# Kernel optimization log

Measured on AMD Instinct MI355X. Metric: run time of the kernel, lower is better.

The kernel has to match this reference:

```python
import jax, jax.numpy as jnp
import numpy as np
from jax import lax

B, CIN, COUT, K, S, P, H, W = 8, 128, 256, 3, 1, 1, 64, 64


def setup_inputs() -> dict:
    key = jax.random.key(0)
    k1, k2, k3, k4, k5 = jax.random.split(key, 5)
    fan_off = CIN * K * K
    fan_dc = CIN * K * K
    return {
        "x": jax.random.normal(k1, (B, CIN, H, W), dtype=jnp.float32),
        # offset-predicting conv: Conv2d(CIN, 2*K*K, K, S, P, padding_mode='reflect')
        "w_off": jax.random.normal(k2, (2 * K * K, CIN, K, K), dtype=jnp.float32) / np.sqrt(fan_off),
        "b_off": jax.random.normal(k3, (2 * K * K,), dtype=jnp.float32) * 0.01,
        # deformable conv weights: DeformConv2d(CIN, COUT, K, S, P)
        "w_dc": jax.random.normal(k4, (COUT, CIN, K, K), dtype=jnp.float32) / np.sqrt(fan_dc),
        "b_dc": jax.random.normal(k5, (COUT,), dtype=jnp.float32) * 0.01,
    }


def _reflect_conv(x, w, b, stride, pad):
    # Conv2d with reflect padding
    xp = jnp.pad(x, ((0, 0), (0, 0), (pad, pad), (pad, pad)), mode="reflect")
    y = lax.conv_general_dilated(xp, w, (stride, stride), "VALID",
                                 dimension_numbers=("NCHW", "OIHW", "NCHW"))
    return y + b[None, :, None, None]


def _deform_conv(x, offset, w, b, k, stride, pad):
    # torchvision DeformConv2d (v1, no mask, 1 offset group)
    Bn, C, Hi, Wi = x.shape
    Ho, Wo = offset.shape[2], offset.shape[3]
    KK = k * k
    # offset layout: [B, 2*KK, Ho, Wo], interleaved (dy, dx) per kernel position
    off = offset.reshape(Bn, KK, 2, Ho, Wo)
    hb = jnp.arange(Ho, dtype=x.dtype) * stride - pad          # base rows
    wb = jnp.arange(Wo, dtype=x.dtype) * stride - pad          # base cols
    ki, kj = jnp.meshgrid(jnp.arange(k, dtype=x.dtype), jnp.arange(k, dtype=x.dtype), indexing="ij")
    ki, kj = ki.reshape(KK), kj.reshape(KK)
    # sampling locations [B, KK, Ho, Wo]
    py = off[:, :, 0] + hb[None, None, :, None] + ki[None, :, None, None]
    px = off[:, :, 1] + wb[None, None, None, :] + kj[None, :, None, None]
    y0 = jnp.floor(py)
    x0 = jnp.floor(px)
    dy = (py - y0).reshape(Bn, 1, -1)
    dx = (px - x0).reshape(Bn, 1, -1)
    y0i = y0.astype(jnp.int32)
    x0i = x0.astype(jnp.int32)
    xf = x.reshape(Bn, C, Hi * Wi)

    def gather(yi, xi):
        valid = (yi >= 0) & (yi < Hi) & (xi >= 0) & (xi < Wi)
        yc = jnp.clip(yi, 0, Hi - 1)
        xc = jnp.clip(xi, 0, Wi - 1)
        idx = (yc * Wi + xc).reshape(Bn, -1)                   # [B, KK*Ho*Wo]
        g = jax.vmap(lambda xb, ib: xb[:, ib])(xf, idx)        # [B, C, KK*Ho*Wo]
        return g * valid.reshape(Bn, 1, -1).astype(x.dtype)

    v00 = gather(y0i, x0i)
    v01 = gather(y0i, x0i + 1)
    v10 = gather(y0i + 1, x0i)
    v11 = gather(y0i + 1, x0i + 1)
    vals = (v00 * (1 - dy) * (1 - dx) + v01 * (1 - dy) * dx
            + v10 * dy * (1 - dx) + v11 * dy * dx)             # [B, C, KK*Ho*Wo]
    cols = vals.reshape(Bn, C, KK, Ho * Wo)
    out = jnp.einsum("bckl,ock->bol", cols, w.reshape(-1, C, KK))
    out = out + b[None, :, None]
    return out.reshape(Bn, -1, Ho, Wo)


def reference(x, w_off, b_off, w_dc, b_dc):
    x_offset = _reflect_conv(x, w_off, b_off, S, P)            # [B, 2*K*K, Ho, Wo]
    # torch.chunk followed by torch.concat is an identity on the offset tensor
    return _deform_conv(x, x_offset, w_dc, b_dc, K, S, P)
```

## Files before the change

### kernel.cpp

```cpp
#include <hip/hip_runtime.h>
#include <hip/hip_fp16.h>

typedef unsigned short u16;
typedef unsigned int   u32;
typedef u32   u32x2  __attribute__((ext_vector_type(2)));
typedef u32   u32x4  __attribute__((ext_vector_type(4)));
typedef short short8 __attribute__((ext_vector_type(8)));
typedef float f32x4  __attribute__((ext_vector_type(4)));
typedef _Float16 half8 __attribute__((ext_vector_type(8)));

__device__ __forceinline__ u16 f2h(float f) { return __half_as_ushort(__float2half(f)); }
__device__ __forceinline__ f32x4 mfma16(short8 a, short8 b, f32x4 c) {
  return __builtin_amdgcn_mfma_f32_16x16x32_f16(
      __builtin_bit_cast(half8, a), __builtin_bit_cast(half8, b), c, 0, 0, 0);
}
__device__ __forceinline__ __half2 h2cast(u32 u) { return __builtin_bit_cast(__half2, u); }
__device__ __forceinline__ int refl(int v) { return v < 0 ? -v : (v > 63 ? 126 - v : v); }

__device__ __forceinline__ void softbar() {
  asm volatile("s_waitcnt lgkmcnt(0)" ::: "memory");
  __builtin_amdgcn_s_barrier();
  asm volatile("" ::: "memory");
}

__global__ __launch_bounds__(256) void prep_fused(const float* __restrict__ x,
                                                  const float* __restrict__ w_dc,
                                                  const float* __restrict__ w_off,
                                                  u16* __restrict__ xh,
                                                  u16* __restrict__ Wl2,
                                                  u16* __restrict__ Wol2) {
  int bid = blockIdx.x;
  int tid = threadIdx.x;
  if (bid < 512) {
    __shared__ float tile[128][65];
    int swz = (bid & 7) * 64 + (bid >> 3);
    int b = swz >> 6, h = swz & 63;
    for (int i = 0; i < 32; ++i) {
      int c = (tid >> 6) + i * 4;
      int w = tid & 63;
      tile[c][w] = x[(((size_t)b * 128 + c) * 64 + h) * 64 + w];
    }
    __syncthreads();
    u16* dst = xh + ((size_t)(b * 64 + h) * 64) * 128;
    for (int j = 0; j < 32; ++j) {
      int c = tid & 127;
      int w = (tid >> 7) + 2 * j;
      dst[w * 128 + c] = f2h(tile[c][w]);
    }
  } else {
    int idx = (bid - 512) * 256 + tid;
    if (idx < 294912) {
      int e = idx & 7, lane = (idx >> 3) & 63, ks = (idx >> 9) & 3;
      int mt = (idx >> 11) & 15, kk = idx >> 15;
      int o = mt * 16 + (lane & 15), c = ks * 32 + (lane >> 4) * 8 + e;
      Wl2[idx] = f2h(w_dc[(o * 128 + c) * 9 + kk]);
    } else {
      int i2 = idx - 294912;
      int e = i2 & 7, lane = (i2 >> 3) & 63, ks = (i2 >> 9) & 3;
      int mt = (i2 >> 11) & 1, kk = i2 >> 12;
      int co = mt * 16 + (lane & 15), c = ks * 32 + (lane >> 4) * 8 + e;
      Wol2[i2] = (co < 18) ? f2h(w_off[(co * 128 + c) * 9 + kk]) : (u16)0;
    }
  }
}

__device__ __forceinline__ void make_entry_lds(u32x4* __restrict__ tbl, int kk,
                                               int ho, int wo, float offy, float offx) {
  int ki = kk / 3, kj = kk - ki * 3;
  float py = offy + (float)(ho + ki - 1);
  float px = offx + (float)(wo + kj - 1);
  float fy0 = floorf(py), fx0 = floorf(px);
  int y0 = (int)fy0, x0 = (int)fx0;
  float fy = py - fy0, fx = px - fx0;
  float w11 = fy * fx, w10 = fy - w11, w01 = fx - w11, w00 = 1.f - fy - fx + w11;
  bool iy0 = (y0 >= 0) & (y0 < 64), iy1 = (y0 >= -1) & (y0 < 63);
  bool ix0 = (x0 >= 0) & (x0 < 64), ix1 = (x0 >= -1) & (x0 < 63);
  int y0c = min(max(y0, 0), 63), x0c = min(max(x0, 0), 63);
  u32 addr00 = (u32)((y0c * 64 + x0c) * 128);
  u32 dx = (x0 >= 0 && x0 < 63) ? 128u : 0u;
  u32 dy = (y0 >= 0 && y0 < 63) ? 8192u : 0u;
  u32 wA = (u32)f2h((iy0 && ix0) ? w00 : 0.f) | ((u32)f2h((iy0 && ix1) ? w01 : 0.f) << 16);
  u32 wB = (u32)f2h((iy1 && ix0) ? w10 : 0.f) | ((u32)f2h((iy1 && ix1) ? w11 : 0.f) << 16);
  u32x4 ent; ent.x = addr00; ent.y = dx | (dy << 16); ent.z = wA; ent.w = wB;
  tbl[kk * 64 + wo] = ent;
}

__global__ __launch_bounds__(512, 4) void deform_fused(
    const u16* __restrict__ xh, const u16* __restrict__ Wl2,
    const u16* __restrict__ Wol2, const float* __restrict__ b_off,
    const float* __restrict__ b_dc, float* __restrict__ out) {
  union SMU {
    u16 slab[3][64][128];
    struct { u16 cols[2][64][128]; u32x4 tbl[576]; } pb;
  };
  __shared__ SMU sm;
  int bid = blockIdx.x;
  int b = bid & 7, ho = bid >> 3;
  int tid = threadIdx.x, lane = tid & 63, wv = tid >> 6;
  int ln15 = lane & 15, kg = lane >> 4;
  const u16* xb = xh + (size_t)b * 524288;

  {
    u32x4 st[6];
#pragma unroll
    for (int i = 0; i < 6; ++i) {
      int T = tid + i * 512;
      int r = T >> 10, w = (T >> 4) & 63, cb = (T & 15) * 8;
      int hr = refl(ho + r - 1);
      st[i] = *(const u32x4*)(xb + (hr * 64 + w) * 128 + cb);
    }
#pragma unroll
    for (int i = 0; i < 6; ++i) {
      int T = tid + i * 512;
      int r = T >> 10, w = (T >> 4) & 63, cb = (T & 15) * 8;
      *(u32x4*)&sm.slab[r][w][cb ^ ((w & 7) << 3)] = st[i];
    }
  }
  __syncthreads();

  int mtA = wv & 1, ntA = wv >> 1;
  int lq = ntA * 16 + ln15;
  f32x4 oacc = {0.f, 0.f, 0.f, 0.f};
  __builtin_amdgcn_s_setprio(1);
#pragma unroll
  for (int kk = 0; kk < 9; ++kk) {
    int ki = kk / 3, kj = kk - ki * 3;
    int j = refl(lq + kj - 1);
    const u16* wb = Wol2 + ((kk * 2 + mtA) * 4) * 512 + lane * 8;
    int sbj = (j & 7) << 3;
#pragma unroll
    for (int ks = 0; ks < 4; ++ks) {
      short8 af = *(const short8*)(wb + ks * 512);
      short8 bf = *(const short8*)&sm.slab[ki][j][(ks * 32 + kg * 8) ^ sbj];
      oacc = mfma16(af, bf, oacc);
    }
  }
  __builtin_amdgcn_s_setprio(0);
  __syncthreads();

  if (mtA == 0) {
    int kkA = 2 * kg, kkB = 2 * kg + 1;
    make_entry_lds(sm.pb.tbl, kkA, ho, lq, oacc[0] + b_off[2 * kkA], oacc[1] + b_off[2 * kkA + 1]);
    make_entry_lds(sm.pb.tbl, kkB, ho, lq, oacc[2] + b_off[2 * kkB], oacc[3] + b_off[2 * kkB + 1]);
  } else if (kg == 0) {
    make_entry_lds(sm.pb.tbl, 8, ho, lq, oacc[0] + b_off[16], oacc[1] + b_off[17]);
  }
  __syncthreads();

  if (wv >= 4) {
    int pt = tid & 255;
    int tl = pt >> 4;
    int tcl = (pt & 15) * 8;
    int swzc = tcl ^ ((tl & 7) << 3);

    u32x4 gv[4][4];
    u32 gwA[4], gwB[4];
    auto gissue = [&](int g) {
#pragma unroll
      for (int i = 0; i < 4; ++i) {
        int l = tl + i * 16;
        u32x4 e = sm.pb.tbl[g * 64 + l];
        gwA[i] = e.z; gwB[i] = e.w;
        const u16* p = xb + e.x + tcl;
        u32 dxv = e.y & 0xffffu, dyv = e.y >> 16;
        gv[i][0] = *(const u32x4*)p;
        gv[i][1] = *(const u32x4*)(p + dxv);
        gv[i][2] = *(const u32x4*)(p + dyv);
        gv[i][3] = *(const u32x4*)(p + dyv + dxv);
      }
    };
    auto gwrite = [&](int dbuf) {
#pragma unroll
      for (int i = 0; i < 4; ++i) {
        int l = tl + i * 16;
        __half2 wA = h2cast(gwA[i]), wB = h2cast(gwB[i]);
        __half2 w00 = __half2half2(wA.x), w01 = __half2half2(wA.y);
        __half2 w10 = __half2half2(wB.x), w11 = __half2half2(wB.y);
        u32x4 pv;
#pragma unroll
        for (int wd = 0; wd < 4; ++wd) {
          __half2 r = __hmul2(h2cast(gv[i][0][wd]), w00);
          r = __hfma2(h2cast(gv[i][1][wd]), w01, r);
          r = __hfma2(h2cast(gv[i][2][wd]), w10, r);
          r = __hfma2(h2cast(gv[i][3][wd]), w11, r);
          pv[wd] = __builtin_bit_cast(u32, r);
        }
        *(u32x4*)&sm.pb.cols[dbuf][l][swzc] = pv;
      }
    };

    gissue(0); gwrite(0);
    gissue(1);
    softbar();
    for (int kk = 0; kk < 9; ++kk) {
      int cur = kk & 1;
      if (kk < 8) gwrite(cur ^ 1);
      if (kk < 7) gissue(kk + 2);
      softbar();
    }
  } else {
    f32x4 acc[4][4];
#pragma unroll
    for (int m = 0; m < 4; ++m)
#pragma unroll
      for (int n = 0; n < 4; ++n) acc[m][n] = (f32x4){0.f, 0.f, 0.f, 0.f};

    int swzb = (ln15 & 7) << 3;
    softbar();
    for (int kk = 0; kk < 9; ++kk) {
      int cur = kk & 1;
      const u16* wb = Wl2 + (size_t)kk * 32768 + lane * 8;
      short8 ac[4], an[4];
#pragma unroll
      for (int m = 0; m < 4; ++m)
        ac[m] = *(const short8*)(wb + (size_t)((wv * 4 + m) * 4) * 512);
#pragma unroll
      for (int ks = 0; ks < 4; ++ks) {
        if (ks < 3) {
#pragma unroll
          for (int m = 0; m < 4; ++m)
            an[m] = *(const short8*)(wb + (size_t)((wv * 4 + m) * 4 + ks + 1) * 512);
        }
        __builtin_amdgcn_s_setprio(1);
#pragma unroll
        for (int nt = 0; nt < 4; ++nt) {
          short8 bf = *(const short8*)&sm.pb.cols[cur][nt * 16 + ln15][(ks * 32 + kg * 8) ^ swzb];
#pragma unroll
          for (int m = 0; m < 4; ++m)
            acc[m][nt] = mfma16(ac[m], bf, acc[m][nt]);
        }
        __builtin_amdgcn_s_setprio(0);
        if (ks < 3) {
#pragma unroll
          for (int m = 0; m < 4; ++m) ac[m] = an[m];
        }
      }
      softbar();
    }

#pragma unroll
    for (int m = 0; m < 4; ++m) {
#pragma unroll
      for (int r = 0; r < 4; ++r) {
        int o = wv * 64 + m * 16 + kg * 4 + r;
        float bias = b_dc[o];
        size_t base = ((size_t)(b * 256 + o)) * 4096 + ho * 64;
#pragma unroll
        for (int nt = 0; nt < 4; ++nt) {
          out[base + nt * 16 + ln15] = acc[m][nt][r] + bias;
        }
      }
    }
  }
}

extern "C" void kernel_launch(void* const* d_in, const int* in_sizes, int n_in,
                              void* d_out, int out_size, void* d_ws, size_t ws_size,
                              hipStream_t stream) {
  const float* x     = (const float*)d_in[0];
  const float* w_off = (const float*)d_in[1];
  const float* b_off = (const float*)d_in[2];
  const float* w_dc  = (const float*)d_in[3];
  const float* b_dc  = (const float*)d_in[4];
  float* out = (float*)d_out;
  char* ws = (char*)d_ws;
  u16* xh   = (u16*)ws;
  u16* Wl2  = (u16*)(ws + 8388608);
  u16* Wol2 = (u16*)(ws + 8388608 + 589824);
  prep_fused  <<<dim3(1808), dim3(256), 0, stream>>>(x, w_dc, w_off, xh, Wl2, Wol2);
  deform_fused<<<dim3(512),  dim3(512), 0, stream>>>(xh, Wl2, Wol2, b_off, b_dc, out);
}
```

Measured before the change: 45.58 us.

## Process two output rows per block with 1024-thread blocks

Each block now covers two output rows instead of one, with 256 blocks of 1024 threads. The 4-row input slab is shared by both rows, which cuts halo reloads from 3 rows per output row to 2. The gather and MFMA warp groups are doubled, and the offset table moves out of the union so one barrier can be dropped. In exchange, 256 blocks is fewer than the CU count on MI355X, which lowers occupancy and parallelism, and the larger blocks use more LDS.

Result: slower. 47.06 us (+3.3%).

```diff
diff --git a/kernel.cpp b/kernel.cpp
--- a/kernel.cpp
+++ b/kernel.cpp
@@ -65,7 +65,8 @@
 }
 
 __device__ __forceinline__ void make_entry_lds(u32x4* __restrict__ tbl, int kk,
-                                               int ho, int wo, float offy, float offx) {
+                                               int ho, int wo, int lq,
+                                               float offy, float offx) {
   int ki = kk / 3, kj = kk - ki * 3;
   float py = offy + (float)(ho + ki - 1);
   float px = offx + (float)(wo + kj - 1);
@@ -82,73 +83,76 @@
   u32 wA = (u32)f2h((iy0 && ix0) ? w00 : 0.f) | ((u32)f2h((iy0 && ix1) ? w01 : 0.f) << 16);
   u32 wB = (u32)f2h((iy1 && ix0) ? w10 : 0.f) | ((u32)f2h((iy1 && ix1) ? w11 : 0.f) << 16);
   u32x4 ent; ent.x = addr00; ent.y = dx | (dy << 16); ent.z = wA; ent.w = wB;
-  tbl[kk * 64 + wo] = ent;
-}
-
-__global__ __launch_bounds__(512, 4) void deform_fused(
+  tbl[kk * 128 + lq] = ent;
+}
+
+__global__ __launch_bounds__(1024, 4) void deform_fused(
     const u16* __restrict__ xh, const u16* __restrict__ Wl2,
     const u16* __restrict__ Wol2, const float* __restrict__ b_off,
     const float* __restrict__ b_dc, float* __restrict__ out) {
-  union SMU {
-    u16 slab[3][64][128];
-    struct { u16 cols[2][64][128]; u32x4 tbl[576]; } pb;
-  };
-  __shared__ SMU sm;
+  __shared__ union SCU {
+    u16 slab[4][64][128];
+    u16 cols[2][128][128];
+  } sc;
+  __shared__ u32x4 tbl[9 * 128];
+
   int bid = blockIdx.x;
-  int b = bid & 7, ho = bid >> 3;
+  int b = bid & 7, t = bid >> 3;
+  int ho0 = t * 2;
   int tid = threadIdx.x, lane = tid & 63, wv = tid >> 6;
   int ln15 = lane & 15, kg = lane >> 4;
   const u16* xb = xh + (size_t)b * 524288;
 
   {
-    u32x4 st[6];
-#pragma unroll
-    for (int i = 0; i < 6; ++i) {
-      int T = tid + i * 512;
+    u32x4 st[4];
+#pragma unroll
+    for (int i = 0; i < 4; ++i) {
+      int T = tid + i * 1024;
       int r = T >> 10, w = (T >> 4) & 63, cb = (T & 15) * 8;
-      int hr = refl(ho + r - 1);
+      int hr = refl(ho0 - 1 + r);
       st[i] = *(const u32x4*)(xb + (hr * 64 + w) * 128 + cb);
     }
 #pragma unroll
-    for (int i = 0; i < 6; ++i) {
-      int T = tid + i * 512;
+    for (int i = 0; i < 4; ++i) {
+      int T = tid + i * 1024;
       int r = T >> 10, w = (T >> 4) & 63, cb = (T & 15) * 8;
-      *(u32x4*)&sm.slab[r][w][cb ^ ((w & 7) << 3)] = st[i];
+      *(u32x4*)&sc.slab[r][w][cb ^ ((w & 7) << 3)] = st[i];
     }
   }
   __syncthreads();
 
-  int mtA = wv & 1, ntA = wv >> 1;
-  int lq = ntA * 16 + ln15;
+  int mtA = wv & 1;
+  int lq = (wv >> 1) * 16 + ln15;
+  int lh = lq >> 6, lw = lq & 63;
   f32x4 oacc = {0.f, 0.f, 0.f, 0.f};
   __builtin_amdgcn_s_setprio(1);
 #pragma unroll
   for (int kk = 0; kk < 9; ++kk) {
     int ki = kk / 3, kj = kk - ki * 3;
-    int j = refl(lq + kj - 1);
+    int j = refl(lw + kj - 1);
+    int row = lh + ki;
     const u16* wb = Wol2 + ((kk * 2 + mtA) * 4) * 512 + lane * 8;
     int sbj = (j & 7) << 3;
 #pragma unroll
     for (int ks = 0; ks < 4; ++ks) {
       short8 af = *(const short8*)(wb + ks * 512);
-      short8 bf = *(const short8*)&sm.slab[ki][j][(ks * 32 + kg * 8) ^ sbj];
+      short8 bf = *(const short8*)&sc.slab[row][j][(ks * 32 + kg * 8) ^ sbj];
       oacc = mfma16(af, bf, oacc);
     }
   }
   __builtin_amdgcn_s_setprio(0);
-  __syncthreads();
 
   if (mtA == 0) {
     int kkA = 2 * kg, kkB = 2 * kg + 1;
-    make_entry_lds(sm.pb.tbl, kkA, ho, lq, oacc[0] + b_off[2 * kkA], oacc[1] + b_off[2 * kkA + 1]);
-    make_entry_lds(sm.pb.tbl, kkB, ho, lq, oacc[2] + b_off[2 * kkB], oacc[3] + b_off[2 * kkB + 1]);
+    make_entry_lds(tbl, kkA, ho0 + lh, lw, lq, oacc[0] + b_off[2 * kkA], oacc[1] + b_off[2 * kkA + 1]);
+    make_entry_lds(tbl, kkB, ho0 + lh, lw, lq, oacc[2] + b_off[2 * kkB], oacc[3] + b_off[2 * kkB + 1]);
   } else if (kg == 0) {
-    make_entry_lds(sm.pb.tbl, 8, ho, lq, oacc[0] + b_off[16], oacc[1] + b_off[17]);
+    make_entry_lds(tbl, 8, ho0 + lh, lw, lq, oacc[0] + b_off[16], oacc[1] + b_off[17]);
   }
   __syncthreads();
 
-  if (wv >= 4) {
-    int pt = tid & 255;
+  if (wv >= 8) {
+    int pt = tid & 511;
     int tl = pt >> 4;
     int tcl = (pt & 15) * 8;
     int swzc = tcl ^ ((tl & 7) << 3);
@@ -158,8 +162,8 @@
     auto gissue = [&](int g) {
 #pragma unroll
       for (int i = 0; i < 4; ++i) {
-        int l = tl + i * 16;
-        u32x4 e = sm.pb.tbl[g * 64 + l];
+        int l = tl + i * 32;
+        u32x4 e = tbl[g * 128 + l];
         gwA[i] = e.z; gwB[i] = e.w;
         const u16* p = xb + e.x + tcl;
         u32 dxv = e.y & 0xffffu, dyv = e.y >> 16;
@@ -172,7 +176,7 @@
     auto gwrite = [&](int dbuf) {
 #pragma unroll
       for (int i = 0; i < 4; ++i) {
-        int l = tl + i * 16;
+        int l = tl + i * 32;
         __half2 wA = h2cast(gwA[i]), wB = h2cast(gwB[i]);
         __half2 w00 = __half2half2(wA.x), w01 = __half2half2(wA.y);
         __half2 w10 = __half2half2(wB.x), w11 = __half2half2(wB.y);
@@ -185,7 +189,7 @@
           r = __hfma2(h2cast(gv[i][3][wd]), w11, r);
           pv[wd] = __builtin_bit_cast(u32, r);
         }
-        *(u32x4*)&sm.pb.cols[dbuf][l][swzc] = pv;
+        *(u32x4*)&sc.cols[dbuf][l][swzc] = pv;
       }
     };
 
@@ -199,6 +203,7 @@
       softbar();
     }
   } else {
+    int cg = wv & 3, lhc = wv >> 2;
     f32x4 acc[4][4];
 #pragma unroll
     for (int m = 0; m < 4; ++m)
@@ -213,18 +218,19 @@
       short8 ac[4], an[4];
 #pragma unroll
       for (int m = 0; m < 4; ++m)
-        ac[m] = *(const short8*)(wb + (size_t)((wv * 4 + m) * 4) * 512);
+        ac[m] = *(const short8*)(wb + (size_t)((cg * 4 + m) * 4) * 512);
 #pragma unroll
       for (int ks = 0; ks < 4; ++ks) {
         if (ks < 3) {
 #pragma unroll
           for (int m = 0; m < 4; ++m)
-            an[m] = *(const short8*)(wb + (size_t)((wv * 4 + m) * 4 + ks + 1) * 512);
+            an[m] = *(const short8*)(wb + (size_t)((cg * 4 + m) * 4 + ks + 1) * 512);
         }
         __builtin_amdgcn_s_setprio(1);
 #pragma unroll
         for (int nt = 0; nt < 4; ++nt) {
-          short8 bf = *(const short8*)&sm.pb.cols[cur][nt * 16 + ln15][(ks * 32 + kg * 8) ^ swzb];
+          int l = lhc * 64 + nt * 16 + ln15;
+          short8 bf = *(const short8*)&sc.cols[cur][l][(ks * 32 + kg * 8) ^ swzb];
 #pragma unroll
           for (int m = 0; m < 4; ++m)
             acc[m][nt] = mfma16(ac[m], bf, acc[m][nt]);
@@ -242,9 +248,9 @@
     for (int m = 0; m < 4; ++m) {
 #pragma unroll
       for (int r = 0; r < 4; ++r) {
-        int o = wv * 64 + m * 16 + kg * 4 + r;
+        int o = cg * 64 + m * 16 + kg * 4 + r;
         float bias = b_dc[o];
-        size_t base = ((size_t)(b * 256 + o)) * 4096 + ho * 64;
+        size_t base = ((size_t)(b * 256 + o)) * 4096 + ho0 * 64 + lhc * 64;
 #pragma unroll
         for (int nt = 0; nt < 4; ++nt) {
           out[base + nt * 16 + ln15] = acc[m][nt][r] + bias;
@@ -268,5 +274,5 @@
   u16* Wl2  = (u16*)(ws + 8388608);
   u16* Wol2 = (u16*)(ws + 8388608 + 589824);
   prep_fused  <<<dim3(1808), dim3(256), 0, stream>>>(x, w_dc, w_off, xh, Wl2, Wol2);
-  deform_fused<<<dim3(512),  dim3(512), 0, stream>>>(xh, Wl2, Wol2, b_off, b_dc, out);
-}
+  deform_fused<<<dim3(256),  dim3(1024), 0, stream>>>(xh, Wl2, Wol2, b_off, b_dc, out);
+}
```

## Pipeline weight fragment loads across kernel positions and coalesce weight-prep reads

Applied to the files above, without the earlier changes.

The MFMA consumer loop is fully unrolled over all 36 (kk, ks) steps with ping-pong A-fragment registers. The next step's weight fragments, including the first slice of the next kernel position, are now fetched while the current MFMAs run, which removes the load stall at the start of each kk. The weight-packing prep kernel now iterates in source order, so reads of w_dc and w_off are coalesced and the writes are scattered into the packed layout. Full unrolling increases code size and register pressure.

Result: slower. 47.05 us (+3.2%).

```diff
diff --git a/kernel.cpp b/kernel.cpp
--- a/kernel.cpp
+++ b/kernel.cpp
@@ -50,16 +50,22 @@
   } else {
     int idx = (bid - 512) * 256 + tid;
     if (idx < 294912) {
-      int e = idx & 7, lane = (idx >> 3) & 63, ks = (idx >> 9) & 3;
-      int mt = (idx >> 11) & 15, kk = idx >> 15;
-      int o = mt * 16 + (lane & 15), c = ks * 32 + (lane >> 4) * 8 + e;
-      Wl2[idx] = f2h(w_dc[(o * 128 + c) * 9 + kk]);
+      int o = idx / 1152;
+      int r = idx - o * 1152;
+      int c = r / 9;
+      int kk = r - c * 9;
+      int lane = (o & 15) | (((c >> 3) & 3) << 4);
+      int widx = (((kk * 16 + (o >> 4)) * 4 + (c >> 5)) * 64 + lane) * 8 + (c & 7);
+      Wl2[widx] = f2h(w_dc[idx]);
     } else {
       int i2 = idx - 294912;
-      int e = i2 & 7, lane = (i2 >> 3) & 63, ks = (i2 >> 9) & 3;
-      int mt = (i2 >> 11) & 1, kk = i2 >> 12;
-      int co = mt * 16 + (lane & 15), c = ks * 32 + (lane >> 4) * 8 + e;
-      Wol2[i2] = (co < 18) ? f2h(w_off[(co * 128 + c) * 9 + kk]) : (u16)0;
+      int o = i2 / 1152;
+      int r = i2 - o * 1152;
+      int c = r / 9;
+      int kk = r - c * 9;
+      int lane = (o & 15) | (((c >> 3) & 3) << 4);
+      int widx = (((kk * 2 + (o >> 4)) * 4 + (c >> 5)) * 64 + lane) * 8 + (c & 7);
+      Wol2[widx] = (o < 18) ? f2h(w_off[i2]) : (u16)0;
     }
   }
 }
@@ -206,36 +212,38 @@
       for (int n = 0; n < 4; ++n) acc[m][n] = (f32x4){0.f, 0.f, 0.f, 0.f};
 
     int swzb = (ln15 & 7) << 3;
+    short8 aA[4], aB[4];
+    const u16* wl0 = Wl2 + lane * 8;
+#pragma unroll
+    for (int m = 0; m < 4; ++m)
+      aA[m] = *(const short8*)(wl0 + (size_t)((wv * 4 + m) * 4) * 512);
+
     softbar();
-    for (int kk = 0; kk < 9; ++kk) {
-      int cur = kk & 1;
-      const u16* wb = Wl2 + (size_t)kk * 32768 + lane * 8;
-      short8 ac[4], an[4];
-#pragma unroll
-      for (int m = 0; m < 4; ++m)
-        ac[m] = *(const short8*)(wb + (size_t)((wv * 4 + m) * 4) * 512);
-#pragma unroll
-      for (int ks = 0; ks < 4; ++ks) {
-        if (ks < 3) {
-#pragma unroll
-          for (int m = 0; m < 4; ++m)
-            an[m] = *(const short8*)(wb + (size_t)((wv * 4 + m) * 4 + ks + 1) * 512);
-        }
-        __builtin_amdgcn_s_setprio(1);
-#pragma unroll
-        for (int nt = 0; nt < 4; ++nt) {
-          short8 bf = *(const short8*)&sm.pb.cols[cur][nt * 16 + ln15][(ks * 32 + kg * 8) ^ swzb];
-#pragma unroll
-          for (int m = 0; m < 4; ++m)
-            acc[m][nt] = mfma16(ac[m], bf, acc[m][nt]);
-        }
-        __builtin_amdgcn_s_setprio(0);
-        if (ks < 3) {
-#pragma unroll
-          for (int m = 0; m < 4; ++m) ac[m] = an[m];
-        }
-      }
-      softbar();
+#pragma unroll
+    for (int G = 0; G < 36; ++G) {
+      const int kk = G >> 2, ks = G & 3;
+      const int cur = kk & 1;
+      __builtin_amdgcn_s_setprio(1);
+#pragma unroll
+      for (int nt = 0; nt < 4; ++nt) {
+        short8 bf = *(const short8*)&sm.pb.cols[cur][nt * 16 + ln15][(ks * 32 + kg * 8) ^ swzb];
+#pragma unroll
+        for (int m = 0; m < 4; ++m) {
+          if (G & 1) acc[m][nt] = mfma16(aB[m], bf, acc[m][nt]);
+          else       acc[m][nt] = mfma16(aA[m], bf, acc[m][nt]);
+        }
+      }
+      __builtin_amdgcn_s_setprio(0);
+      if (G < 35) {
+        const int nk = (G + 1) >> 2, ns = (G + 1) & 3;
+        const u16* wb = wl0 + (size_t)nk * 32768;
+#pragma unroll
+        for (int m = 0; m < 4; ++m) {
+          short8 v = *(const short8*)(wb + (size_t)((wv * 4 + m) * 4 + ns) * 512);
+          if (G & 1) aA[m] = v; else aB[m] = v;
+        }
+      }
+      if (ks == 3) softbar();
     }
 
 #pragma unroll
```
